# Optimization experiments

Hardware: AMD Instinct MI355X
Metric: run time of the kernel (lower is better)

The kernel has to match this reference:

```python
import jax, jax.numpy as jnp
import numpy as np

B = 512      # batch
H = 64       # latent_dim == GRU hidden size
F = 32       # n_features
S = 2048     # seq_len
NEG_SLOPE = 0.01  # nn.LeakyReLU default


def setup_inputs() -> dict:
    key = jax.random.key(0)
    ks = jax.random.split(key, 14)

    def p(k, shape, scale=0.1):
        return jax.random.normal(k, shape, dtype=jnp.float32) * scale

    return {
        "noise": jax.random.normal(ks[0], (B, H), dtype=jnp.float32),
        # GRU forward direction (layer 0): weight_ih_l0, weight_hh_l0, biases
        "W_ih_f": p(ks[1], (3 * H, H)),
        "W_hh_f": p(ks[2], (3 * H, H)),
        "b_ih_f": p(ks[3], (3 * H,)),
        "b_hh_f": p(ks[4], (3 * H,)),
        # GRU backward direction (layer 0 reverse)
        "W_ih_b": p(ks[5], (3 * H, H)),
        "W_hh_b": p(ks[6], (3 * H, H)),
        "b_ih_b": p(ks[7], (3 * H,)),
        "b_hh_b": p(ks[8], (3 * H,)),
        # latent_linear: Linear(2H -> H)
        "W_lat": p(ks[9], (H, 2 * H)),
        "b_lat": p(ks[10], (H,)),
        # output_linear: Linear(H -> F)
        "W_out": p(ks[11], (F, H)),
        "b_out": p(ks[12], (F,)),
    }


def _leaky(x):
    return jnp.where(x >= 0, x, NEG_SLOPE * x)


def _gru_cell(x, h, W_ih, W_hh, b_ih, b_hh):
    # PyTorch GRU cell: gates ordered (r, z, n)
    gi = x @ W_ih.T + b_ih          # (B, 3H)
    gh = h @ W_hh.T + b_hh          # (B, 3H)
    i_r, i_z, i_n = jnp.split(gi, 3, axis=-1)
    h_r, h_z, h_n = jnp.split(gh, 3, axis=-1)
    r = jax.nn.sigmoid(i_r + h_r)
    z = jax.nn.sigmoid(i_z + h_z)
    n = jnp.tanh(i_n + r * h_n)
    return (1.0 - z) * n + z * h


def reference(noise, W_ih_f, W_hh_f, b_ih_f, b_hh_f,
              W_ih_b, W_hh_b, b_ih_b, b_hh_b,
              W_lat, b_lat, W_out, b_out):
    # hidden_state = noise.repeat((D*n_layers,1,1)) -> both directions start at noise
    batch = noise.shape[0]

    def step(carry, _):
        x, hf, hb = carry
        # GRU on a length-1 sequence: each direction does one cell update;
        # output timestep = concat(fwd_out, bwd_out)
        hf2 = _gru_cell(x, hf, W_ih_f, W_hh_f, b_ih_f, b_hh_f)
        hb2 = _gru_cell(x, hb, W_ih_b, W_hh_b, b_ih_b, b_hh_b)
        out = jnp.concatenate([hf2, hb2], axis=-1)        # (B, 2H)
        lat = _leaky(out @ W_lat.T + b_lat)               # (B, H)
        return (lat, hf2, hb2), lat

    x0 = jnp.zeros((batch, H), dtype=noise.dtype)
    _, ys = jax.lax.scan(step, (x0, noise, noise), None, length=S)
    seq = jnp.transpose(ys, (1, 0, 2))   # (B, S, H)
    seq = _leaky(seq)                    # second LeakyReLU as in the original
    out = jax.nn.sigmoid(seq @ W_out.T + b_out)  # (B, S, F)
    return out
```

## Files before the change

kernel.cpp:

```cpp
#include <hip/hip_runtime.h>
#include <hip/hip_bf16.h>


#define NBATCH 512
#define NH 64
#define NS 2048
#define NF 32
#define MROW 16
#define LDH 72

typedef short s16x8 __attribute__((ext_vector_type(8)));
typedef float f32x4 __attribute__((ext_vector_type(4)));

#define MFMA(a, b, c) __builtin_amdgcn_mfma_f32_16x16x32_bf16((a), (b), (c), 0, 0, 0)

#define NLOG2E  (-1.4426950408889634f)
#define N2LOG2E (-2.8853900817779268f)

#define PIN(x) __asm__("" : "+v"(x))

__device__ __forceinline__ void bar_lds() {
    __asm__ volatile("s_waitcnt lgkmcnt(0)\n\ts_barrier" ::: "memory");
}

__device__ __forceinline__ short f2bf(float f) {
    return (short)((__float_as_uint(f) + 0x8000u) >> 16);
}

__device__ __forceinline__ f32x4 v_exp2(f32x4 a) {
    f32x4 r;
#pragma unroll
    for (int i = 0; i < 4; ++i) r[i] = __builtin_amdgcn_exp2f(a[i]);
    return r;
}

__device__ __forceinline__ f32x4 v_rcp(f32x4 a) {
    f32x4 r;
#pragma unroll
    for (int i = 0; i < 4; ++i) r[i] = __builtin_amdgcn_rcpf(a[i]);
    return r;
}

__device__ __forceinline__ f32x4 v_lk(f32x4 a) {
    f32x4 b = a * 0.01f;
    f32x4 r;
#pragma unroll
    for (int i = 0; i < 4; ++i) r[i] = fmaxf(a[i], b[i]);
    return r;
}

__device__ __forceinline__ f32x4 v_sigm(f32x4 a) {
    return v_rcp(v_exp2(a * NLOG2E) + 1.0f);
}

__device__ __forceinline__ int2 pk4bf(f32x4 v) {
    union { __hip_bfloat162 b; int i; } lo, hi;
    float2 a; a.x = v[0]; a.y = v[1];
    float2 b; b.x = v[2]; b.y = v[3];
    lo.b = __float22bfloat162_rn(a);
    hi.b = __float22bfloat162_rn(b);
    int2 r; r.x = lo.i; r.y = hi.i;
    return r;
}

__device__ __forceinline__ s16x8 bfragW(const float* __restrict__ W, int ldk,
                                        int row, int kf, int quad) {
    const float* p = W + (size_t)row * ldk + kf * 32 + quad * 8;
    s16x8 r;
#pragma unroll
    for (int i = 0; i < 8; ++i) r[i] = f2bf(p[i]);
    return r;
}

__device__ __forceinline__ f32x4 bias4(const float* __restrict__ p) {
    const float4 v = *(const float4*)p;
    f32x4 r = {v.x, v.y, v.z, v.w};
    return r;
}

__global__ __launch_bounds__(1024)
__attribute__((amdgpu_waves_per_eu(4, 4)))
void grugan_kernel(const float* __restrict__ noise,
                   const float* __restrict__ Wihf, const float* __restrict__ Whhf,
                   const float* __restrict__ bihf, const float* __restrict__ bhhf,
                   const float* __restrict__ Wihb, const float* __restrict__ Whhb,
                   const float* __restrict__ bihb, const float* __restrict__ bhhb,
                   const float* __restrict__ Wlat, const float* __restrict__ blat,
                   const float* __restrict__ Wout, const float* __restrict__ bout,
                   float* __restrict__ out)
{
    __shared__ __align__(16) short Xs[2][MROW][LDH];
    __shared__ __align__(16) short X2s[2][MROW][LDH];
    __shared__ __align__(16) short Hs[2][2][MROW][LDH];

    const int tid  = threadIdx.x;
    const int wave = tid >> 6;
    const int lane = tid & 63;
    const int n    = lane & 15;
    const int quad = lane >> 4;
    const int row0 = blockIdx.x * MROW;

    for (int idx = tid; idx < MROW * LDH; idx += 1024) (&Xs[0][0][0])[idx] = 0;
    f32x4 hreg = {0.f, 0.f, 0.f, 0.f};
    const int gdir = wave >> 2;
    const int gjq  = (wave & 3) * 16 + quad * 4;
    if (wave < 8) {
        const float4 nz = *(const float4*)&noise[(size_t)(row0 + n) * NH + gjq];
        hreg[0] = nz.x; hreg[1] = nz.y; hreg[2] = nz.z; hreg[3] = nz.w;
        *(int2*)&Hs[0][gdir][n][gjq] = pk4bf(hreg);
    }
    __syncthreads();

    if (wave < 8) {
        const int dir  = gdir;
        const int cb   = wave & 3;
        const int jrow = cb * 16 + n;
        const int jq   = gjq;
        const float* Wih = dir ? Wihb : Wihf;
        const float* Whh = dir ? Whhb : Whhf;
        const float* bih = dir ? bihb : bihf;
        const float* bhh = dir ? bhhb : bhhf;

        s16x8 wir0 = bfragW(Wih, NH,   0 + jrow, 0, quad);
        s16x8 wir1 = bfragW(Wih, NH,   0 + jrow, 1, quad);
        s16x8 wiz0 = bfragW(Wih, NH,  64 + jrow, 0, quad);
        s16x8 wiz1 = bfragW(Wih, NH,  64 + jrow, 1, quad);
        s16x8 win0 = bfragW(Wih, NH, 128 + jrow, 0, quad);
        s16x8 win1 = bfragW(Wih, NH, 128 + jrow, 1, quad);
        s16x8 whr0 = bfragW(Whh, NH,   0 + jrow, 0, quad);
        s16x8 whr1 = bfragW(Whh, NH,   0 + jrow, 1, quad);
        s16x8 whz0 = bfragW(Whh, NH,  64 + jrow, 0, quad);
        s16x8 whz1 = bfragW(Whh, NH,  64 + jrow, 1, quad);
        s16x8 whn0 = bfragW(Whh, NH, 128 + jrow, 0, quad);
        s16x8 whn1 = bfragW(Whh, NH, 128 + jrow, 1, quad);
        f32x4 initR, initZ;
        {
            f32x4 a = bias4(&bih[jq]),      b = bias4(&bhh[jq]);
            initR = a + b;
            f32x4 c = bias4(&bih[64 + jq]), d = bias4(&bhh[64 + jq]);
            initZ = c + d;
        }
        f32x4 initN1 = bias4(&bih[128 + jq]);
        f32x4 initN2 = bias4(&bhh[128 + jq]);
        PIN(wir0); PIN(wir1); PIN(wiz0); PIN(wiz1); PIN(win0); PIN(win1);
        PIN(whr0); PIN(whr1); PIN(whz0); PIN(whz1); PIN(whn0); PIN(whn1);
        PIN(initR); PIN(initZ); PIN(initN1); PIN(initN2);

        f32x4 accR, accZ, accN2;
        {
            s16x8 ha0 = *(const s16x8*)&Hs[0][dir][n][quad * 8];
            s16x8 ha1 = *(const s16x8*)&Hs[0][dir][n][32 + quad * 8];
            accR  = MFMA(whr0, ha0, initR);  accR  = MFMA(whr1, ha1, accR);
            accZ  = MFMA(whz0, ha0, initZ);  accZ  = MFMA(whz1, ha1, accZ);
            accN2 = MFMA(whn0, ha0, initN2); accN2 = MFMA(whn1, ha1, accN2);
        }

#define GSTEP(HB) do {                                                          \
        s16x8 xa0 = *(const s16x8*)&Xs[HB][n][quad * 8];                        \
        s16x8 xa1 = *(const s16x8*)&Xs[HB][n][32 + quad * 8];                   \
        accR = MFMA(wir0, xa0, accR);   accR = MFMA(wir1, xa1, accR);           \
        accZ = MFMA(wiz0, xa0, accZ);   accZ = MFMA(wiz1, xa1, accZ);           \
        f32x4 accN1 = MFMA(win0, xa0, initN1);                                  \
        accN1 = MFMA(win1, xa1, accN1);                                         \
        f32x4 eR = v_exp2(accR * NLOG2E);                                       \
        f32x4 rr = v_rcp(eR + 1.0f);                                            \
        f32x4 u  = accN1 + rr * accN2;                                          \
        f32x4 eU = v_exp2(u * N2LOG2E);                                         \
        f32x4 eZ = v_exp2(accZ * NLOG2E);                                       \
        f32x4 numer = (eZ + hreg) + eU * (hreg - eZ);                           \
        f32x4 denom = (eU + 1.0f) * (eZ + 1.0f);                                \
        hreg = numer * v_rcp(denom);                                            \
        *(int2*)&Hs[(HB) ^ 1][dir][n][jq] = pk4bf(hreg);                        \
        bar_lds();                                      \
        {                                                                       \
            s16x8 ha0 = *(const s16x8*)&Hs[(HB) ^ 1][dir][n][quad * 8];         \
            s16x8 ha1 = *(const s16x8*)&Hs[(HB) ^ 1][dir][n][32 + quad * 8];    \
            accR  = MFMA(whr0, ha0, initR);  accR  = MFMA(whr1, ha1, accR);     \
            accZ  = MFMA(whz0, ha0, initZ);  accZ  = MFMA(whz1, ha1, accZ);     \
            accN2 = MFMA(whn0, ha0, initN2); accN2 = MFMA(whn1, ha1, accN2);    \
        }                                                                       \
        bar_lds();                                      \
    } while (0)

        for (int t = 0; t < NS; t += 2) {
            GSTEP(0);
            GSTEP(1);
        }
#undef GSTEP
    } else if (wave < 12) {
        const int lt = wave & 3;
        const int nq = lt * 16 + quad * 4;
        s16x8 wl0 = bfragW(Wlat, 2 * NH, lt * 16 + n, 0, quad);
        s16x8 wl1 = bfragW(Wlat, 2 * NH, lt * 16 + n, 1, quad);
        s16x8 wl2 = bfragW(Wlat, 2 * NH, lt * 16 + n, 2, quad);
        s16x8 wl3 = bfragW(Wlat, 2 * NH, lt * 16 + n, 3, quad);
        f32x4 initL = bias4(&blat[lt * 16 + quad * 4]);
        PIN(wl0); PIN(wl1); PIN(wl2); PIN(wl3); PIN(initL);
        const f32x4 Z4 = {0.f, 0.f, 0.f, 0.f};

#define LSTEP(HB) do {                                                          \
        bar_lds();                                      \
        s16x8 fa0 = *(const s16x8*)&Hs[(HB) ^ 1][0][n][quad * 8];               \
        s16x8 fa1 = *(const s16x8*)&Hs[(HB) ^ 1][0][n][32 + quad * 8];          \
        s16x8 ba0 = *(const s16x8*)&Hs[(HB) ^ 1][1][n][quad * 8];               \
        s16x8 ba1 = *(const s16x8*)&Hs[(HB) ^ 1][1][n][32 + quad * 8];          \
        f32x4 c1 = MFMA(wl0, fa0, initL);                                       \
        c1 = MFMA(wl1, fa1, c1);                                                \
        f32x4 c2 = MFMA(wl2, ba0, Z4);                                          \
        c2 = MFMA(wl3, ba1, c2);                                                \
        f32x4 la = v_lk(c1 + c2);                                               \
        *(int2*)&Xs[(HB) ^ 1][n][nq]  = pk4bf(la);                              \
        *(int2*)&X2s[(HB) ^ 1][n][nq] = pk4bf(v_lk(la));                        \
        bar_lds();                                      \
    } while (0)

        for (int t = 0; t < NS; t += 2) {
            LSTEP(0);
            LSTEP(1);
        }
#undef LSTEP
    } else if (wave < 14) {
        const int f0 = (wave & 1) * 16;
        s16x8 wo0 = bfragW(Wout, NH, f0 + n, 0, quad);
        s16x8 wo1 = bfragW(Wout, NH, f0 + n, 1, quad);
        f32x4 initO = bias4(&bout[f0 + quad * 4]);
        PIN(wo0); PIN(wo1); PIN(initO);
        float* const orow = out + (size_t)(row0 + n) * (NS * NF) + f0 + quad * 4;

#define OSTEP(HB, T) do {                                                       \
        if ((T) >= 1) {                                                         \
            s16x8 p0 = *(const s16x8*)&X2s[HB][n][quad * 8];                    \
            s16x8 p1 = *(const s16x8*)&X2s[HB][n][32 + quad * 8];               \
            f32x4 po = MFMA(wo0, p0, initO);                                    \
            po = MFMA(wo1, p1, po);                                             \
            *(f32x4*)(orow + (size_t)((T) - 1) * NF) = v_sigm(po);              \
        }                                                                       \
        bar_lds();                                                      \
        bar_lds();                                                      \
    } while (0)

        for (int t = 0; t < NS; t += 2) {
            OSTEP(0, t);
            OSTEP(1, t + 1);
        }
#undef OSTEP

        s16x8 p0 = *(const s16x8*)&X2s[0][n][quad * 8];
        s16x8 p1 = *(const s16x8*)&X2s[0][n][32 + quad * 8];
        f32x4 po = MFMA(wo0, p0, initO);
        po = MFMA(wo1, p1, po);
        *(f32x4*)(orow + (size_t)(NS - 1) * NF) = v_sigm(po);
    } else {
#pragma unroll 1
        for (int i = 0; i < 2 * NS; ++i) bar_lds();
    }
}

extern "C" void kernel_launch(void* const* d_in, const int* in_sizes, int n_in,
                              void* d_out, int out_size, void* d_ws, size_t ws_size,
                              hipStream_t stream) {
    const float* noise = (const float*)d_in[0];
    const float* Wihf  = (const float*)d_in[1];
    const float* Whhf  = (const float*)d_in[2];
    const float* bihf  = (const float*)d_in[3];
    const float* bhhf  = (const float*)d_in[4];
    const float* Wihb  = (const float*)d_in[5];
    const float* Whhb  = (const float*)d_in[6];
    const float* bihb  = (const float*)d_in[7];
    const float* bhhb  = (const float*)d_in[8];
    const float* Wlat  = (const float*)d_in[9];
    const float* blat  = (const float*)d_in[10];
    const float* Wout  = (const float*)d_in[11];
    const float* bout  = (const float*)d_in[12];

    grugan_kernel<<<dim3(NBATCH / MROW), dim3(1024), 0, stream>>>(
        noise, Wihf, Whhf, bihf, bhhf, Wihb, Whhb, bihb, bhhb,
        Wlat, blat, Wout, bout, (float*)d_out);
}
```

Measured before the change: 1.621 ms.

## Merge latent and output waves into two waves, shrink block to 640 threads

Folds the latent-linear work (previously 4 waves) and the output-projection work (previously 2 waves) into 2 waves. Each of those waves computes two latent column tiles and one output tile per step. The 2 idle barrier-only waves are removed, so each block drops from 16 to 10 waves. Fewer waves taking part in each per-step barrier should cut barrier cost and scheduling pressure on the serial recurrence. The cost is more MFMA and LDS work per step on the latent path, which sits on the critical path between GRU steps.

```diff
diff --git a/kernel.cpp b/kernel.cpp
--- a/kernel.cpp
+++ b/kernel.cpp
@@ -78,8 +78,8 @@
     return r;
 }
 
-__global__ __launch_bounds__(1024)
-__attribute__((amdgpu_waves_per_eu(4, 4)))
+__global__ __launch_bounds__(640)
+__attribute__((amdgpu_waves_per_eu(3, 3)))
 void grugan_kernel(const float* __restrict__ noise,
                    const float* __restrict__ Wihf, const float* __restrict__ Whhf,
                    const float* __restrict__ bihf, const float* __restrict__ bhhf,
@@ -100,7 +100,7 @@
     const int quad = lane >> 4;
     const int row0 = blockIdx.x * MROW;
 
-    for (int idx = tid; idx < MROW * LDH; idx += 1024) (&Xs[0][0][0])[idx] = 0;
+    for (int idx = tid; idx < MROW * LDH; idx += 640) (&Xs[0][0][0])[idx] = 0;
     f32x4 hreg = {0.f, 0.f, 0.f, 0.f};
     const int gdir = wave >> 2;
     const int gjq  = (wave & 3) * 16 + quad * 4;
@@ -187,47 +187,33 @@
             GSTEP(1);
         }
 #undef GSTEP
-    } else if (wave < 12) {
-        const int lt = wave & 3;
-        const int nq = lt * 16 + quad * 4;
-        s16x8 wl0 = bfragW(Wlat, 2 * NH, lt * 16 + n, 0, quad);
-        s16x8 wl1 = bfragW(Wlat, 2 * NH, lt * 16 + n, 1, quad);
-        s16x8 wl2 = bfragW(Wlat, 2 * NH, lt * 16 + n, 2, quad);
-        s16x8 wl3 = bfragW(Wlat, 2 * NH, lt * 16 + n, 3, quad);
-        f32x4 initL = bias4(&blat[lt * 16 + quad * 4]);
-        PIN(wl0); PIN(wl1); PIN(wl2); PIN(wl3); PIN(initL);
-        const f32x4 Z4 = {0.f, 0.f, 0.f, 0.f};
-
-#define LSTEP(HB) do {                                                          \
-        bar_lds();                                      \
-        s16x8 fa0 = *(const s16x8*)&Hs[(HB) ^ 1][0][n][quad * 8];               \
-        s16x8 fa1 = *(const s16x8*)&Hs[(HB) ^ 1][0][n][32 + quad * 8];          \
-        s16x8 ba0 = *(const s16x8*)&Hs[(HB) ^ 1][1][n][quad * 8];               \
-        s16x8 ba1 = *(const s16x8*)&Hs[(HB) ^ 1][1][n][32 + quad * 8];          \
-        f32x4 c1 = MFMA(wl0, fa0, initL);                                       \
-        c1 = MFMA(wl1, fa1, c1);                                                \
-        f32x4 c2 = MFMA(wl2, ba0, Z4);                                          \
-        c2 = MFMA(wl3, ba1, c2);                                                \
-        f32x4 la = v_lk(c1 + c2);                                               \
-        *(int2*)&Xs[(HB) ^ 1][n][nq]  = pk4bf(la);                              \
-        *(int2*)&X2s[(HB) ^ 1][n][nq] = pk4bf(v_lk(la));                        \
-        bar_lds();                                      \
-    } while (0)
-
-        for (int t = 0; t < NS; t += 2) {
-            LSTEP(0);
-            LSTEP(1);
-        }
-#undef LSTEP
-    } else if (wave < 14) {
-        const int f0 = (wave & 1) * 16;
+    } else {
+        const int lw  = wave - 8;
+        const int lt0 = lw * 2;
+        const int nq0 = lt0 * 16 + quad * 4;
+        const int nq1 = nq0 + 16;
+        s16x8 wlA0 = bfragW(Wlat, 2 * NH, lt0 * 16 + n, 0, quad);
+        s16x8 wlA1 = bfragW(Wlat, 2 * NH, lt0 * 16 + n, 1, quad);
+        s16x8 wlA2 = bfragW(Wlat, 2 * NH, lt0 * 16 + n, 2, quad);
+        s16x8 wlA3 = bfragW(Wlat, 2 * NH, lt0 * 16 + n, 3, quad);
+        s16x8 wlB0 = bfragW(Wlat, 2 * NH, lt0 * 16 + 16 + n, 0, quad);
+        s16x8 wlB1 = bfragW(Wlat, 2 * NH, lt0 * 16 + 16 + n, 1, quad);
+        s16x8 wlB2 = bfragW(Wlat, 2 * NH, lt0 * 16 + 16 + n, 2, quad);
+        s16x8 wlB3 = bfragW(Wlat, 2 * NH, lt0 * 16 + 16 + n, 3, quad);
+        f32x4 initL0 = bias4(&blat[lt0 * 16 + quad * 4]);
+        f32x4 initL1 = bias4(&blat[lt0 * 16 + 16 + quad * 4]);
+        const int f0 = lw * 16;
         s16x8 wo0 = bfragW(Wout, NH, f0 + n, 0, quad);
         s16x8 wo1 = bfragW(Wout, NH, f0 + n, 1, quad);
         f32x4 initO = bias4(&bout[f0 + quad * 4]);
-        PIN(wo0); PIN(wo1); PIN(initO);
+        PIN(wlA0); PIN(wlA1); PIN(wlA2); PIN(wlA3);
+        PIN(wlB0); PIN(wlB1); PIN(wlB2); PIN(wlB3);
+        PIN(initL0); PIN(initL1); PIN(wo0); PIN(wo1); PIN(initO);
+        const f32x4 Z4 = {0.f, 0.f, 0.f, 0.f};
         float* const orow = out + (size_t)(row0 + n) * (NS * NF) + f0 + quad * 4;
 
-#define OSTEP(HB, T) do {                                                       \
+#define LSTEP(HB, T) do {                                                       \
+                     \
         if ((T) >= 1) {                                                         \
             s16x8 p0 = *(const s16x8*)&X2s[HB][n][quad * 8];                    \
             s16x8 p1 = *(const s16x8*)&X2s[HB][n][32 + quad * 8];               \
@@ -235,24 +221,41 @@
             po = MFMA(wo1, p1, po);                                             \
             *(f32x4*)(orow + (size_t)((T) - 1) * NF) = v_sigm(po);              \
         }                                                                       \
-        bar_lds();                                                      \
-        bar_lds();                                                      \
+        bar_lds();                                      \
+        {                                                                       \
+            s16x8 fa0 = *(const s16x8*)&Hs[(HB) ^ 1][0][n][quad * 8];           \
+            s16x8 fa1 = *(const s16x8*)&Hs[(HB) ^ 1][0][n][32 + quad * 8];      \
+            s16x8 ba0 = *(const s16x8*)&Hs[(HB) ^ 1][1][n][quad * 8];           \
+            s16x8 ba1 = *(const s16x8*)&Hs[(HB) ^ 1][1][n][32 + quad * 8];      \
+            f32x4 c1 = MFMA(wlA0, fa0, initL0);                                 \
+            c1 = MFMA(wlA1, fa1, c1);                                           \
+            f32x4 c2 = MFMA(wlA2, ba0, Z4);                                     \
+            c2 = MFMA(wlA3, ba1, c2);                                           \
+            f32x4 c3 = MFMA(wlB0, fa0, initL1);                                 \
+            c3 = MFMA(wlB1, fa1, c3);                                           \
+            f32x4 c4 = MFMA(wlB2, ba0, Z4);                                     \
+            c4 = MFMA(wlB3, ba1, c4);                                           \
+            f32x4 la0 = v_lk(c1 + c2);                                          \
+            f32x4 la1 = v_lk(c3 + c4);                                          \
+            *(int2*)&Xs[(HB) ^ 1][n][nq0]  = pk4bf(la0);                        \
+            *(int2*)&X2s[(HB) ^ 1][n][nq0] = pk4bf(v_lk(la0));                  \
+            *(int2*)&Xs[(HB) ^ 1][n][nq1]  = pk4bf(la1);                        \
+            *(int2*)&X2s[(HB) ^ 1][n][nq1] = pk4bf(v_lk(la1));                  \
+        }                                                                       \
+        bar_lds();                                      \
     } while (0)
 
         for (int t = 0; t < NS; t += 2) {
-            OSTEP(0, t);
-            OSTEP(1, t + 1);
-        }
-#undef OSTEP
+            LSTEP(0, t);
+            LSTEP(1, t + 1);
+        }
+#undef LSTEP
 
         s16x8 p0 = *(const s16x8*)&X2s[0][n][quad * 8];
         s16x8 p1 = *(const s16x8*)&X2s[0][n][32 + quad * 8];
         f32x4 po = MFMA(wo0, p0, initO);
         po = MFMA(wo1, p1, po);
         *(f32x4*)(orow + (size_t)(NS - 1) * NF) = v_sigm(po);
-    } else {
-#pragma unroll 1
-        for (int i = 0; i < 2 * NS; ++i) bar_lds();
     }
 }
 
@@ -273,7 +276,7 @@
     const float* Wout  = (const float*)d_in[11];
     const float* bout  = (const float*)d_in[12];
 
-    grugan_kernel<<<dim3(NBATCH / MROW), dim3(1024), 0, stream>>>(
+    grugan_kernel<<<dim3(NBATCH / MROW), dim3(640), 0, stream>>>(
         noise, Wihf, Whhf, bihf, bhhf, Wihb, Whhb, bihb, bhhb,
         Wlat, blat, Wout, bout, (float*)d_out);
 }
```

After: 1.784 ms. 10.1% more time.
